# Optimization experiments

Hardware: AMD Instinct MI355X
Metric: run time of the kernel (lower is better)

The kernel has to match this reference:

```python
import jax, jax.numpy as jnp
import numpy as np
import math

D_MODEL = 1024
D_INNER = 2048
N_HEADS = 8
D_STATE = 64
D_CONV = 4
CHUNK = 64
HEAD_DIM = D_INNER // N_HEADS
EPS = 1.1920929e-07  # torch RMSNorm default eps = finfo(fp32).eps


def _rms(x, g):
    return x * jax.lax.rsqrt(jnp.mean(x * x, axis=-1, keepdims=True) + EPS) * g


def setup_inputs() -> dict:
    key = jax.random.key(0)
    ks = jax.random.split(key, 8)
    B, S = 32, 256
    proj_out = 2 * D_INNER + 2 * N_HEADS * D_STATE + N_HEADS  # 5128
    s = 0.02
    lambdas = [0.999, 0.995, 0.99, 0.98, 0.95, 0.9, 0.8, 0.7]
    A_log = jnp.log(jnp.asarray([-math.log(l) for l in lambdas], jnp.float32))
    return {
        "hidden": jax.random.normal(ks[0], (B, S, D_MODEL), jnp.float32),
        "W_in": jax.random.normal(ks[1], (proj_out, D_MODEL), jnp.float32) * s,
        "conv_w": jax.random.normal(ks[2], (D_INNER, 1, D_CONV), jnp.float32) * 0.2,
        "conv_b": jax.random.normal(ks[3], (D_INNER,), jnp.float32) * 0.02,
        "W_dt": jax.random.normal(ks[4], (D_INNER, N_HEADS), jnp.float32) * 0.1,
        "b_dt": jax.random.normal(ks[5], (D_INNER,), jnp.float32) * 0.1,
        "A_log": A_log,
        "D": jnp.ones((N_HEADS,), jnp.float32),
        "W_out": jax.random.normal(ks[6], (D_MODEL, D_INNER), jnp.float32) * s,
        "g_in": jnp.ones((D_MODEL,), jnp.float32),
        "g_out": jnp.ones((D_INNER,), jnp.float32),
    }


def reference(hidden, W_in, conv_w, conv_b, W_dt, b_dt, A_log, D, W_out, g_in, g_out):
    B, S, _ = hidden.shape
    residual = hidden
    h = _rms(hidden, g_in)
    proj = h @ W_in.T  # [B,S,5128]
    o1, o2 = D_INNER, 2 * D_INNER
    o3 = o2 + N_HEADS * D_STATE
    o4 = o3 + N_HEADS * D_STATE
    z = proj[..., :o1]
    x = proj[..., o1:o2]
    Bf = proj[..., o2:o3]
    Cf = proj[..., o3:o4]
    dt_raw = proj[..., o4:]
    # causal depthwise conv1d (pad left d_conv-1, trim to S)
    xt = jnp.transpose(x, (0, 2, 1))  # [B, d_inner, S]
    xc = jax.lax.conv_general_dilated(
        xt, conv_w, (1,), [(D_CONV - 1, 0)],
        feature_group_count=D_INNER, dimension_numbers=("NCH", "OIH", "NCH"))
    x = jax.nn.silu(jnp.transpose(xc + conv_b[None, :, None], (0, 2, 1)))
    # dt: project 8 -> d_inner then mean over head_dim -> per-head dt
    dt = dt_raw @ W_dt.T + b_dt  # [B,S,d_inner]
    dt_h = jax.nn.softplus(dt.reshape(B, S, N_HEADS, HEAD_DIM).mean(-1))  # non-TTT path (S<384)
    Bs = Bf.reshape(B, S, N_HEADS, D_STATE)
    Cs = Cf.reshape(B, S, N_HEADS, D_STATE)
    x_h = x.reshape(B, S, N_HEADS, HEAD_DIM)
    # chunked SSD scan
    A = -jnp.exp(A_log)  # [H]
    nC, L = S // CHUNK, CHUNK
    xck = x_h.reshape(B, nC, L, N_HEADS, HEAD_DIM)
    Bck = Bs.reshape(B, nC, L, N_HEADS, D_STATE)
    Cck = Cs.reshape(B, nC, L, N_HEADS, D_STATE)
    logA = dt_h.reshape(B, nC, L, N_HEADS) * A  # [B,c,L,H]
    lcs = jnp.cumsum(logA, axis=2)
    lcs_t = jnp.transpose(lcs, (0, 1, 3, 2))  # [B,c,H,L]
    tril = jnp.tril(jnp.ones((L, L), bool))
    M = jnp.where(tril, jnp.exp(lcs_t[..., :, None] - lcs_t[..., None, :]), 0.0)  # [B,c,H,L,L]
    # intra-chunk: sum_{s<=l,n} C[l,n] M[l,s] B[s,n] x[s,d]
    G = jnp.einsum("bclhn,bcshn->bchls", Cck, Bck)
    intra = jnp.einsum("bchls,bcshd->bclhd", G * M, xck)
    # per-chunk state contributions and decays
    Mlast = jnp.exp(lcs_t[..., -1:] - lcs_t)  # [B,c,H,L] decay from step s to chunk end
    states = jnp.einsum("bchs,bcshn,bcshd->bchdn", Mlast, Bck, xck)  # [B,c,H,hD,N]
    tdec = jnp.exp(lcs[:, :, -1, :])  # [B,c,H]
    def step(hst, inp):
        td, st = inp
        return td[..., None, None] * hst + st, hst
    init = jnp.zeros((B, N_HEADS, HEAD_DIM, D_STATE), x.dtype)
    _, h0 = jax.lax.scan(step, init, (jnp.moveaxis(tdec, 1, 0), jnp.moveaxis(states, 1, 0)))
    # inter-chunk: decay(l) * C[l] . h_start
    inter = jnp.exp(lcs)[..., None] * jnp.einsum("bclhn,cbhdn->bclhd", Cck, h0)
    y = (intra + inter).reshape(B, S, N_HEADS, HEAD_DIM) + x_h * D[None, None, :, None]
    y = y.reshape(B, S, D_INNER) * jax.nn.silu(z)
    y = _rms(y, g_out)
    return residual + y @ W_out.T
```

## Files before the change

kernel.cpp:

```cpp
#include <hip/hip_runtime.h>
#include <hip/hip_bf16.h>
#include <math.h>

typedef __hip_bfloat16 bf16;
typedef __attribute__((ext_vector_type(8))) short short8;
typedef __attribute__((ext_vector_type(4))) float f32x4;

#define AS1 __attribute__((address_space(1)))
#define AS3 __attribute__((address_space(3)))

#define D_MODEL 1024
#define D_INNER 2048
#define N_HEADS 8
#define D_STATE 64
#define CHUNK 64
#define HEAD_DIM 256
#define NCHUNK 4
#define BATCH 32
#define SEQ 256
#define ROWS (BATCH*SEQ)
#define PROJ_N 5128
#define PROJ_NPAD 5376
#define O1 D_INNER
#define O2 (2*D_INNER)
#define O3 (O2 + N_HEADS*D_STATE)
#define O4 (O3 + N_HEADS*D_STATE)
#define EPSF 1.1920929e-07f

__device__ __forceinline__ float silu_f(float x){ return x / (1.0f + expf(-x)); }
__device__ __forceinline__ float b2f(bf16 v){ return __bfloat162float(v); }
__device__ __forceinline__ bf16  f2b(float v){ return __float2bfloat16(v); }
__device__ __forceinline__ short f2s(float v){ bf16 b = __float2bfloat16(v); union{bf16 b; short s;} u; u.b=b; return u.s; }
__device__ __forceinline__ float s2f(short v){ union{short s; bf16 b;} u; u.s=v; return __bfloat162float(u.b); }

__device__ __forceinline__ void gl16(const void* g, void* l){
    __builtin_amdgcn_global_load_lds((const AS1 void*)g, (AS3 void*)l, 16, 0, 0);
}

__device__ __forceinline__ float block_sum_256(float v){
    __shared__ float sm[4];
    #pragma unroll
    for (int o = 32; o > 0; o >>= 1) v += __shfl_down(v, o, 64);
    int lane = threadIdx.x & 63, w = threadIdx.x >> 6;
    if (lane == 0) sm[w] = v;
    __syncthreads();
    return sm[0] + sm[1] + sm[2] + sm[3];
}

__global__ __launch_bounds__(256) void k_rms_in(const float* __restrict__ x,
                                                const float* __restrict__ g,
                                                bf16* __restrict__ out){
    int row = blockIdx.x, t = threadIdx.x;
    const float4* xr = (const float4*)(x + (size_t)row * D_MODEL);
    float4 v = xr[t];
    float ss = v.x*v.x + v.y*v.y + v.z*v.z + v.w*v.w;
    ss = block_sum_256(ss);
    float sc = rsqrtf(ss * (1.0f/(float)D_MODEL) + EPSF);
    float4 gv = ((const float4*)g)[t];
    union { ushort4 u; bf16 b[4]; } o;
    o.b[0] = f2b(v.x*sc*gv.x); o.b[1] = f2b(v.y*sc*gv.y);
    o.b[2] = f2b(v.z*sc*gv.z); o.b[3] = f2b(v.w*sc*gv.w);
    ((ushort4*)(out + (size_t)row * D_MODEL))[t] = o.u;
}

__global__ __launch_bounds__(256) void k_cvt_pad(const float* __restrict__ in,
                                                 bf16* __restrict__ out,
                                                 int n_in, int n_out){
    int i = (blockIdx.x * 256 + threadIdx.x) * 4;
    if (i >= n_out) return;
    union { ushort4 u; bf16 b[4]; } o;
    if (i + 3 < n_in){
        float4 v = *(const float4*)(in + i);
        o.b[0]=f2b(v.x); o.b[1]=f2b(v.y); o.b[2]=f2b(v.z); o.b[3]=f2b(v.w);
    } else {
        #pragma unroll
        for (int j = 0; j < 4; j++) o.b[j] = f2b((i+j < n_in) ? in[i+j] : 0.f);
    }
    *(ushort4*)(out + i) = o.u;
}


__device__ __forceinline__ short8 ld32(const short* base, int row, int g){
    int sr = row >> 1;
    int e8 = (((row & 1) << 2) | g) ^ (sr & 7);
    return *(const short8*)(base + sr*64 + e8*8);
}

__device__ __forceinline__ void stage_u(const bf16* __restrict__ Ag,
                                        const bf16* __restrict__ Bg,
                                        int K, size_t bm, size_t bn, int t,
                                        short* buf, int j){
    const int tid = threadIdx.x;
    const int wid = tid >> 6;
    int cidx = j*512 + tid;
    int srow = cidx >> 3, s8 = cidx & 7;
    int eff = s8 ^ (srow & 7);
    int grow = srow*2 + (eff >> 2);
    int gcol = t*32 + (eff & 3)*8;
    const bf16* src = (grow < 256)
        ? Ag + (bm + grow) * (size_t)K + gcol
        : Bg + (bn + grow - 256) * (size_t)K + gcol;
    gl16(src, buf + (size_t)(j*512 + wid*64)*8);
}

#define MFMA_BF16(A_,B_,C_) __builtin_amdgcn_mfma_f32_16x16x32_bf16(A_,B_,C_,0,0,0)

__device__ __forceinline__ void gemm_main(const bf16* __restrict__ Ag,
                                          const bf16* __restrict__ Bg,
                                          int K, size_t bm, size_t bn,
                                          short* lds, f32x4 (&acc)[4][4]){
    constexpr int TILE = 384*32;
    const int NT = K >> 5;
    const int lane = threadIdx.x & 63;
    const int wid = threadIdx.x >> 6;
    const int wm = wid >> 1, wn = wid & 1;
    const int fr = lane & 15, g = lane >> 4;

    #pragma unroll
    for (int j = 0; j < 3; j++) stage_u(Ag, Bg, K, bm, bn, 0, lds, j);
    #pragma unroll
    for (int j = 0; j < 3; j++) stage_u(Ag, Bg, K, bm, bn, 1, lds + TILE, j);
    asm volatile("s_waitcnt vmcnt(3)" ::: "memory");
    __builtin_amdgcn_sched_barrier(0);
    __builtin_amdgcn_s_barrier();
    __builtin_amdgcn_sched_barrier(0);

    int cur = 0;
    for (int t = 0; t < NT; t++){
        short* buf = lds + cur*TILE;
        int sg = cur + 2; if (sg >= 3) sg -= 3;
        short* stg = lds + sg*TILE;
        short8 a[4], b[4];
        #pragma unroll
        for (int m = 0; m < 4; m++) a[m] = ld32(buf, wm*64 + m*16 + fr, g);
        #pragma unroll
        for (int n = 0; n < 4; n++) b[n] = ld32(buf, 256 + wn*64 + n*16 + fr, g);
        if (t + 2 < NT){
            stage_u(Ag, Bg, K, bm, bn, t+2, stg, 0);
            stage_u(Ag, Bg, K, bm, bn, t+2, stg, 1);
            stage_u(Ag, Bg, K, bm, bn, t+2, stg, 2);
        }
        __builtin_amdgcn_s_setprio(1);
        #pragma unroll
        for (int m = 0; m < 4; m++)
            #pragma unroll
            for (int n = 0; n < 4; n++)
                acc[m][n] = MFMA_BF16(a[m], b[n], acc[m][n]);
        __builtin_amdgcn_s_setprio(0);
        __builtin_amdgcn_sched_barrier(0);
        if (t + 2 < NT)      asm volatile("s_waitcnt vmcnt(3)" ::: "memory");
        else if (t + 1 < NT) asm volatile("s_waitcnt vmcnt(0)" ::: "memory");
        __builtin_amdgcn_sched_barrier(0);
        __builtin_amdgcn_s_barrier();
        __builtin_amdgcn_sched_barrier(0);
        cur = cur + 1 == 3 ? 0 : cur + 1;
    }
}

__global__ __launch_bounds__(512, 4) void k_gemm1_g(const bf16* __restrict__ A,
                                                    const bf16* __restrict__ B,
                                                    bf16* __restrict__ z,
                                                    bf16* __restrict__ xp,
                                                    bf16* __restrict__ Bc,
                                                    bf16* __restrict__ Cc,
                                                    float* __restrict__ dtr){
    extern __shared__ short lds[];
    int wg = (blockIdx.x & 7)*168 + (blockIdx.x >> 3);
    int grp = wg / 192, rem = wg % 192;
    int nt_ = grp*6 + rem % 6;
    int mt_ = rem / 6;
    size_t bm = (size_t)mt_ * 256;
    size_t bn = (size_t)nt_ * 128;
    f32x4 acc[4][4] = {};
    gemm_main(A, B, D_MODEL, bm, bn, lds, acc);
    const int lane = threadIdx.x & 63;
    const int wid = threadIdx.x >> 6;
    const int wm = wid >> 1, wn = wid & 1;
    int cr = (lane >> 4)*4, cc = lane & 15;
    #pragma unroll
    for (int m = 0; m < 4; m++){
        size_t r0 = bm + wm*64 + m*16 + cr;
        #pragma unroll
        for (int n = 0; n < 4; n++){
            int c = (int)bn + wn*64 + n*16 + cc;
            #pragma unroll
            for (int j = 0; j < 4; j++){
                float v = acc[m][n][j];
                size_t r = r0 + j;
                if (c < O1)            z  [r * D_INNER + c]        = f2b(v);
                else if (c < O2)       xp [r * D_INNER + (c - O1)] = f2b(v);
                else if (c < O3)       Bc [r * 512 + (c - O2)]     = f2b(v);
                else if (c < O4)       Cc [r * 512 + (c - O3)]     = f2b(v);
                else if (c < PROJ_N)   dtr[r * 8 + (c - O4)]       = v;
            }
        }
    }
}

__global__ __launch_bounds__(512, 4) void k_gemm2_g(const bf16* __restrict__ A,
                                                    const bf16* __restrict__ B,
                                                    const float* __restrict__ res,
                                                    float* __restrict__ C){
    extern __shared__ short lds[];
    int wg = (blockIdx.x & 7)*32 + (blockIdx.x >> 3);
    size_t bm = (size_t)(wg >> 3) * 256;
    size_t bn = (size_t)(wg & 7) * 128;
    f32x4 acc[4][4] = {};
    gemm_main(A, B, D_INNER, bm, bn, lds, acc);
    const int lane = threadIdx.x & 63;
    const int wid = threadIdx.x >> 6;
    const int wm = wid >> 1, wn = wid & 1;
    int cr = (lane >> 4)*4, cc = lane & 15;
    #pragma unroll
    for (int m = 0; m < 4; m++){
        size_t r0 = bm + wm*64 + m*16 + cr;
        #pragma unroll
        for (int n = 0; n < 4; n++){
            size_t c = bn + wn*64 + n*16 + cc;
            #pragma unroll
            for (int j = 0; j < 4; j++){
                size_t r = r0 + j;
                C[r * D_MODEL + c] = acc[m][n][j] + res[r * D_MODEL + c];
            }
        }
    }
}

__global__ __launch_bounds__(256) void k_conv_silu(const bf16* __restrict__ xp,
                                                   const float* __restrict__ cw,
                                                   const float* __restrict__ cb,
                                                   bf16* __restrict__ xout){
    int b = blockIdx.x;
    int c = blockIdx.y * 256 + threadIdx.x;
    int s0 = blockIdx.z * 32;
    float w0 = cw[c*4+0], w1 = cw[c*4+1], w2 = cw[c*4+2], w3 = cw[c*4+3];
    float bias = cb[c];
    const bf16* ib = xp + (size_t)b * SEQ * D_INNER + c;
    bf16* ob = xout + (size_t)b * SEQ * D_INNER + c;
    float x0 = 0.f, x1 = 0.f, x2 = 0.f;
    if (s0 >= 3){
        x0 = b2f(ib[(size_t)(s0-3) * D_INNER]);
        x1 = b2f(ib[(size_t)(s0-2) * D_INNER]);
        x2 = b2f(ib[(size_t)(s0-1) * D_INNER]);
    }
    #pragma unroll 4
    for (int s = s0; s < s0 + 32; s++){
        float x3 = b2f(ib[(size_t)s * D_INNER]);
        float a = x0*w0 + x1*w1 + x2*w2 + x3*w3 + bias;
        ob[(size_t)s * D_INNER] = f2b(silu_f(a));
        x0 = x1; x1 = x2; x2 = x3;
    }
}

__global__ __launch_bounds__(64) void k_dt_lcs(const float* __restrict__ dtr,
                                               const float* __restrict__ W_dt,
                                               const float* __restrict__ b_dt,
                                               const float* __restrict__ A_log,
                                               float* __restrict__ lcs,
                                               float* __restrict__ tdec){
    __shared__ float sm[80];
    __shared__ float la[CHUNK][N_HEADS];
    int bc = blockIdx.x;
    int l = threadIdx.x;
    {
        int h = l >> 3, k = l & 7;
        float s = 0.f;
        for (int d = 0; d < HEAD_DIM; d++) s += W_dt[(size_t)(h*HEAD_DIM + d) * N_HEADS + k];
        sm[l] = s * (1.0f/(float)HEAD_DIM);
        if (l < 8){
            float sb = 0.f;
            for (int d = 0; d < HEAD_DIM; d++) sb += b_dt[l*HEAD_DIM + d];
            sm[64 + l] = sb * (1.0f/(float)HEAD_DIM);
            sm[72 + l] = -expf(A_log[l]);
        }
    }
    __syncthreads();
    const float* dr = dtr + (size_t)(bc*CHUNK + l) * 8;
    float d0 = dr[0], d1 = dr[1], d2 = dr[2], d3 = dr[3];
    float d4 = dr[4], d5 = dr[5], d6 = dr[6], d7 = dr[7];
    #pragma unroll
    for (int h = 0; h < 8; h++){
        float dt = sm[64+h]
                 + d0*sm[h*8+0] + d1*sm[h*8+1] + d2*sm[h*8+2] + d3*sm[h*8+3]
                 + d4*sm[h*8+4] + d5*sm[h*8+5] + d6*sm[h*8+6] + d7*sm[h*8+7];
        float sp = (dt > 20.f) ? dt : log1pf(expf(dt));
        la[l][h] = sp * sm[72+h];
    }
    __syncthreads();
    float out[8];
    #pragma unroll
    for (int h = 0; h < 8; h++) out[h] = 0.f;
    for (int l2 = 0; l2 <= l; l2++){
        #pragma unroll
        for (int h = 0; h < 8; h++) out[h] += la[l2][h];
    }
    float* lo = lcs + (size_t)(bc*CHUNK + l) * N_HEADS;
    #pragma unroll
    for (int h = 0; h < 8; h++) lo[h] = out[h];
    if (l == 63){
        #pragma unroll
        for (int h = 0; h < 8; h++) tdec[bc*N_HEADS + h] = expf(out[h]);
    }
}

#define LB   0
#define LC   4096
#define LGM  8192
#define LXT  12800
#define LSH  29184
#define LF   45568
#define LDS_BYTES 91904

__device__ __forceinline__ short8 frag_sw(const short* arr, int r, int k){
    return *(const short8*)(arr + r*64 + (k ^ ((r&7)<<3)));
}

__global__ __launch_bounds__(256, 1) void k_ssm(const bf16* __restrict__ Bc,
                                                const bf16* __restrict__ Cc,
                                                bf16* xg,
                                                const float* __restrict__ lcs,
                                                const float* __restrict__ tdec,
                                                const float* __restrict__ Dv){
    extern __shared__ short lds[];
    short* Blds  = lds + LB;
    short* Clds  = lds + LC;
    short* GMlds = lds + LGM;
    short* XTlds = lds + LXT;
    short* Shr   = lds + LSH;
    float* el = (float*)(lds + LF);
    float* ml = el + 64;
    float* ee = el + 128;

    const int tid = threadIdx.x;
    const int lane = tid & 63;
    const int wid = tid >> 6;
    const int fr = lane & 15;
    const int fk = (lane >> 4) * 8;
    const int r0 = (lane >> 4) * 4;
    const int b = blockIdx.x >> 3, h = blockIdx.x & 7;
    const float Dh = Dv[h];

    f32x4 carry[4][4] = {};

    for (int c = 0; c < NCHUNK; c++){
        const int bc = b*NCHUNK + c;
        __syncthreads();
        #pragma unroll
        for (int i = 0; i < 2; i++){
            int slot = i*256 + tid;
            int s = slot >> 3, u = slot & 7;
            size_t rb = (size_t)(bc*CHUNK + s) * 512 + h*64 + ((u ^ (s&7)) * 8);
            gl16(Bc + rb, Blds + slot*8);
            gl16(Cc + rb, Clds + slot*8);
        }
        #pragma unroll
        for (int i = 0; i < 8; i++){
            int slot = i*256 + tid;
            int s = slot >> 5, ck = slot & 31;
            gl16(xg + (size_t)(bc*CHUNK + s) * D_INNER + h*HEAD_DIM + ck*8, Shr + slot*8);
        }
        if (tid < 64) el[tid] = lcs[(size_t)(bc*CHUNK + tid) * N_HEADS + h];
        __syncthreads();
        if (tid < 64){
            float e63 = el[63];
            ml[tid] = expf(e63 - el[tid]);
            ee[tid] = expf(el[tid]);
        }
        #pragma unroll
        for (int i = 0; i < 8; i++){
            short8 t8;
            #pragma unroll
            for (int j = 0; j < 8; j++) t8[j] = Shr[(i*8 + j)*HEAD_DIM + tid];
            *(short8*)(XTlds + tid*64 + ((i*8) ^ ((tid&7)<<3))) = t8;
        }
        __syncthreads();
        {
            f32x4 accg[4] = {};
            #pragma unroll
            for (int kk = 0; kk < 2; kk++){
                short8 a = frag_sw(Clds, wid*16 + fr, kk*32 + fk);
                #pragma unroll
                for (int nt = 0; nt < 4; nt++){
                    short8 bb = frag_sw(Blds, nt*16 + fr, kk*32 + fk);
                    accg[nt] = __builtin_amdgcn_mfma_f32_16x16x32_bf16(a, bb, accg[nt], 0, 0, 0);
                }
            }
            #pragma unroll
            for (int nt = 0; nt < 4; nt++){
                int s = nt*16 + fr;
                float els = el[s];
                #pragma unroll
                for (int j = 0; j < 4; j++){
                    int l = wid*16 + r0 + j;
                    float f = (s <= l) ? expf(el[l] - els) : 0.f;
                    GMlds[l*72 + s] = f2s(accg[nt][j] * f);
                }
            }
            int crow = wid*16 + (lane >> 2), cq = lane & 3;
            float fe = ee[crow];
            #pragma unroll
            for (int half = 0; half < 2; half++){
                short8 v = *(short8*)(Clds + crow*64 + cq*16 + half*8);
                #pragma unroll
                for (int j = 0; j < 8; j++) v[j] = f2s(s2f(v[j]) * fe);
                *(short8*)(Clds + crow*64 + cq*16 + half*8) = v;
            }
        }
        #pragma unroll
        for (int mt = 0; mt < 4; mt++)
            #pragma unroll
            for (int nt = 0; nt < 4; nt++)
                #pragma unroll
                for (int j = 0; j < 4; j++){
                    int d = wid*64 + mt*16 + r0 + j;
                    int n = nt*16 + fr;
                    Shr[d*64 + (n ^ ((d&7)<<3))] = f2s(carry[mt][nt][j]);
                }
        float btv[16];
        {
            int bn_ = tid & 63, bq = tid >> 6;
            #pragma unroll
            for (int i = 0; i < 16; i++){
                int s = bq*16 + i;
                btv[i] = s2f(Blds[s*64 + (bn_ ^ ((s&7)<<3))]) * ml[s];
            }
        }
        __syncthreads();
        {
            int bn_ = tid & 63, bq = tid >> 6;
            #pragma unroll
            for (int i = 0; i < 16; i++){
                int s = bq*16 + i;
                Blds[bn_*64 + (s ^ ((bn_&7)<<3))] = f2s(btv[i]);
            }
        }
        {
            f32x4 accy[4][4] = {};
            #pragma unroll
            for (int kk = 0; kk < 2; kk++){
                short8 ag[4], ae[4], bx[4], bh[4];
                #pragma unroll
                for (int mt = 0; mt < 4; mt++){
                    ag[mt] = *(const short8*)(GMlds + (mt*16 + fr)*72 + kk*32 + fk);
                    ae[mt] = frag_sw(Clds, mt*16 + fr, kk*32 + fk);
                }
                #pragma unroll
                for (int nt = 0; nt < 4; nt++){
                    int d = wid*64 + nt*16 + fr;
                    bx[nt] = frag_sw(XTlds, d, kk*32 + fk);
                    bh[nt] = frag_sw(Shr,  d, kk*32 + fk);
                }
                #pragma unroll
                for (int mt = 0; mt < 4; mt++)
                    #pragma unroll
                    for (int nt = 0; nt < 4; nt++){
                        accy[mt][nt] = __builtin_amdgcn_mfma_f32_16x16x32_bf16(ag[mt], bx[nt], accy[mt][nt], 0, 0, 0);
                        accy[mt][nt] = __builtin_amdgcn_mfma_f32_16x16x32_bf16(ae[mt], bh[nt], accy[mt][nt], 0, 0, 0);
                    }
            }
            #pragma unroll
            for (int mt = 0; mt < 4; mt++)
                #pragma unroll
                for (int nt = 0; nt < 4; nt++){
                    int d = wid*64 + nt*16 + fr;
                    #pragma unroll
                    for (int j = 0; j < 4; j++){
                        int l = mt*16 + r0 + j;
                        float xv = s2f(XTlds[d*64 + (l ^ ((d&7)<<3))]);
                        xg[(size_t)(bc*CHUNK + l) * D_INNER + h*HEAD_DIM + d] = f2b(accy[mt][nt][j] + xv*Dh);
                    }
                }
        }
        __syncthreads();
        {
            f32x4 accs[4][4] = {};
            #pragma unroll
            for (int kk = 0; kk < 2; kk++){
                short8 ax[4], bt[4];
                #pragma unroll
                for (int mt = 0; mt < 4; mt++)
                    ax[mt] = frag_sw(XTlds, wid*64 + mt*16 + fr, kk*32 + fk);
                #pragma unroll
                for (int nt = 0; nt < 4; nt++)
                    bt[nt] = frag_sw(Blds, nt*16 + fr, kk*32 + fk);
                #pragma unroll
                for (int mt = 0; mt < 4; mt++)
                    #pragma unroll
                    for (int nt = 0; nt < 4; nt++)
                        accs[mt][nt] = __builtin_amdgcn_mfma_f32_16x16x32_bf16(ax[mt], bt[nt], accs[mt][nt], 0, 0, 0);
            }
            float td = tdec[bc*N_HEADS + h];
            #pragma unroll
            for (int mt = 0; mt < 4; mt++)
                #pragma unroll
                for (int nt = 0; nt < 4; nt++)
                    carry[mt][nt] = td * carry[mt][nt] + accs[mt][nt];
        }
    }
}

__global__ __launch_bounds__(256) void k_gate_rms(const bf16* __restrict__ y,
                                                  const bf16* __restrict__ z,
                                                  const float* __restrict__ g,
                                                  bf16* __restrict__ yn){
    int row = blockIdx.x, t = threadIdx.x;
    union { uint4 u; bf16 b[8]; } yv, zv, ov;
    yv.u = ((const uint4*)(y + (size_t)row * D_INNER))[t];
    zv.u = ((const uint4*)(z + (size_t)row * D_INNER))[t];
    float v[8];
    float ss = 0.f;
    #pragma unroll
    for (int i = 0; i < 8; i++){
        float a = b2f(yv.b[i]);
        float q = b2f(zv.b[i]);
        v[i] = a * silu_f(q);
        ss += v[i]*v[i];
    }
    ss = block_sum_256(ss);
    float sc = rsqrtf(ss * (1.0f/(float)D_INNER) + EPSF);
    const float4* g4 = (const float4*)g;
    float4 ga = g4[2*t], gb = g4[2*t+1];
    float gg[8] = {ga.x,ga.y,ga.z,ga.w,gb.x,gb.y,gb.z,gb.w};
    #pragma unroll
    for (int i = 0; i < 8; i++) ov.b[i] = f2b(v[i]*sc*gg[i]);
    ((uint4*)(yn + (size_t)row * D_INNER))[t] = ov.u;
}

extern "C" void kernel_launch(void* const* d_in, const int* in_sizes, int n_in,
                              void* d_out, int out_size, void* d_ws, size_t ws_size,
                              hipStream_t stream){
    const float* hidden = (const float*)d_in[0];
    const float* W_in   = (const float*)d_in[1];
    const float* conv_w = (const float*)d_in[2];
    const float* conv_b = (const float*)d_in[3];
    const float* W_dt   = (const float*)d_in[4];
    const float* b_dt   = (const float*)d_in[5];
    const float* A_log  = (const float*)d_in[6];
    const float* Dv     = (const float*)d_in[7];
    const float* W_out  = (const float*)d_in[8];
    const float* g_in   = (const float*)d_in[9];
    const float* g_out  = (const float*)d_in[10];

    char* ws = (char*)d_ws;
    bf16*  z    = (bf16*)(ws + 0);
    bf16*  xp   = (bf16*)(ws + 33554432);
    bf16*  x    = (bf16*)(ws + 67108864);
    bf16*  Bc   = (bf16*)(ws + 100663296);
    bf16*  Cc   = (bf16*)(ws + 109051904);
    float* dtr  = (float*)(ws + 117440512);
    float* lcs  = (float*)(ws + 117702656);
    float* tdec = (float*)(ws + 117964800);
    bf16*  Wb   = (bf16*)(ws + 117969408);
    bf16*  hnb  = (bf16*)(ws + 128979456);
    bf16*  yn   = xp;

    k_rms_in<<<ROWS, 256, 0, stream>>>(hidden, g_in, hnb);
    k_cvt_pad<<<(PROJ_NPAD*D_MODEL/4 + 255)/256, 256, 0, stream>>>(W_in, Wb, PROJ_N*D_MODEL, PROJ_NPAD*D_MODEL);
    hipFuncSetAttribute((const void*)k_gemm1_g, hipFuncAttributeMaxDynamicSharedMemorySize, 73728);
    k_gemm1_g<<<(ROWS/256)*(PROJ_NPAD/128), 512, 73728, stream>>>(hnb, Wb, z, xp, Bc, Cc, dtr);
    k_conv_silu<<<dim3(BATCH, D_INNER/256, SEQ/32), 256, 0, stream>>>(xp, conv_w, conv_b, x);
    k_dt_lcs<<<BATCH*NCHUNK, 64, 0, stream>>>(dtr, W_dt, b_dt, A_log, lcs, tdec);
    hipFuncSetAttribute((const void*)k_ssm, hipFuncAttributeMaxDynamicSharedMemorySize, LDS_BYTES);
    k_ssm<<<BATCH*N_HEADS, 256, LDS_BYTES, stream>>>(Bc, Cc, x, lcs, tdec, Dv);
    k_gate_rms<<<ROWS, 256, 0, stream>>>(x, z, g_out, yn);
    k_cvt_pad<<<(D_MODEL*D_INNER/4 + 255)/256, 256, 0, stream>>>(W_out, Wb, D_MODEL*D_INNER, D_MODEL*D_INNER);
    hipFuncSetAttribute((const void*)k_gemm2_g, hipFuncAttributeMaxDynamicSharedMemorySize, 73728);
    k_gemm2_g<<<(ROWS/256)*(D_MODEL/128), 512, 73728, stream>>>(yn, Wb, hidden, (float*)d_out);
}
```

Before: 266.8 us.

## Fuse gating into SSM, fold RMS scale into GEMM2, merge weight conversions

The silu(z) gate moves into the SSM epilogue. The output RMSNorm is split into two parts: a row-scale kernel that only computes rsqrt per row, and a g_out multiply folded into the bf16 W_out conversion, so the per-row scale is applied in the GEMM2 epilogue. This removes one full read-modify-write pass over the normalized activations. Both weight conversions are merged into one launch, and GEMM2 switches to a 4-stage LDS pipeline (prefetch depth 3) with more shared memory, which may lower occupancy. The sum of squares is now taken over bf16-rounded gated values, which slightly changes numerics.

```diff
diff --git a/kernel.cpp b/kernel.cpp
--- a/kernel.cpp
+++ b/kernel.cpp
@@ -63,20 +63,33 @@
     ((ushort4*)(out + (size_t)row * D_MODEL))[t] = o.u;
 }
 
-__global__ __launch_bounds__(256) void k_cvt_pad(const float* __restrict__ in,
-                                                 bf16* __restrict__ out,
-                                                 int n_in, int n_out){
+#define N1 (PROJ_NPAD*D_MODEL)
+__global__ __launch_bounds__(256) void k_cvt_both(const float* __restrict__ W_in,
+                                                  const float* __restrict__ W_out,
+                                                  const float* __restrict__ g_out,
+                                                  bf16* __restrict__ Wb1,
+                                                  bf16* __restrict__ Wb2){
     int i = (blockIdx.x * 256 + threadIdx.x) * 4;
-    if (i >= n_out) return;
     union { ushort4 u; bf16 b[4]; } o;
-    if (i + 3 < n_in){
-        float4 v = *(const float4*)(in + i);
-        o.b[0]=f2b(v.x); o.b[1]=f2b(v.y); o.b[2]=f2b(v.z); o.b[3]=f2b(v.w);
+    if (i < N1){
+        int n_in = PROJ_N*D_MODEL;
+        if (i + 3 < n_in){
+            float4 v = *(const float4*)(W_in + i);
+            o.b[0]=f2b(v.x); o.b[1]=f2b(v.y); o.b[2]=f2b(v.z); o.b[3]=f2b(v.w);
+        } else {
+            #pragma unroll
+            for (int j = 0; j < 4; j++) o.b[j] = f2b((i+j < n_in) ? W_in[i+j] : 0.f);
+        }
+        *(ushort4*)(Wb1 + i) = o.u;
     } else {
-        #pragma unroll
-        for (int j = 0; j < 4; j++) o.b[j] = f2b((i+j < n_in) ? in[i+j] : 0.f);
-    }
-    *(ushort4*)(out + i) = o.u;
+        int k2 = i - N1;
+        if (k2 < D_MODEL*D_INNER){
+            float4 v = *(const float4*)(W_out + k2);
+            float4 gv = *(const float4*)(g_out + (k2 & (D_INNER-1)));
+            o.b[0]=f2b(v.x*gv.x); o.b[1]=f2b(v.y*gv.y); o.b[2]=f2b(v.z*gv.z); o.b[3]=f2b(v.w*gv.w);
+            *(ushort4*)(Wb2 + k2) = o.u;
+        }
+    }
 }
 
 
@@ -154,6 +167,59 @@
         __builtin_amdgcn_s_barrier();
         __builtin_amdgcn_sched_barrier(0);
         cur = cur + 1 == 3 ? 0 : cur + 1;
+    }
+}
+
+__device__ __forceinline__ void gemm_main_r4(const bf16* __restrict__ Ag,
+                                             const bf16* __restrict__ Bg,
+                                             int K, size_t bm, size_t bn,
+                                             short* lds, f32x4 (&acc)[4][4]){
+    constexpr int TILE = 384*32;
+    const int NT = K >> 5;
+    const int lane = threadIdx.x & 63;
+    const int wid = threadIdx.x >> 6;
+    const int wm = wid >> 1, wn = wid & 1;
+    const int fr = lane & 15, g = lane >> 4;
+
+    #pragma unroll
+    for (int p = 0; p < 3; p++)
+        #pragma unroll
+        for (int j = 0; j < 3; j++) stage_u(Ag, Bg, K, bm, bn, p, lds + p*TILE, j);
+    asm volatile("s_waitcnt vmcnt(6)" ::: "memory");
+    __builtin_amdgcn_sched_barrier(0);
+    __builtin_amdgcn_s_barrier();
+    __builtin_amdgcn_sched_barrier(0);
+
+    int cur = 0;
+    for (int t = 0; t < NT; t++){
+        short* buf = lds + cur*TILE;
+        int sg = cur + 3; if (sg >= 4) sg -= 4;
+        short* stg = lds + sg*TILE;
+        short8 a[4], b[4];
+        #pragma unroll
+        for (int m = 0; m < 4; m++) a[m] = ld32(buf, wm*64 + m*16 + fr, g);
+        #pragma unroll
+        for (int n = 0; n < 4; n++) b[n] = ld32(buf, 256 + wn*64 + n*16 + fr, g);
+        if (t + 3 < NT){
+            stage_u(Ag, Bg, K, bm, bn, t+3, stg, 0);
+            stage_u(Ag, Bg, K, bm, bn, t+3, stg, 1);
+            stage_u(Ag, Bg, K, bm, bn, t+3, stg, 2);
+        }
+        __builtin_amdgcn_s_setprio(1);
+        #pragma unroll
+        for (int m = 0; m < 4; m++)
+            #pragma unroll
+            for (int n = 0; n < 4; n++)
+                acc[m][n] = MFMA_BF16(a[m], b[n], acc[m][n]);
+        __builtin_amdgcn_s_setprio(0);
+        __builtin_amdgcn_sched_barrier(0);
+        if (t + 3 < NT)      asm volatile("s_waitcnt vmcnt(6)" ::: "memory");
+        else if (t + 2 < NT) asm volatile("s_waitcnt vmcnt(3)" ::: "memory");
+        else if (t + 1 < NT) asm volatile("s_waitcnt vmcnt(0)" ::: "memory");
+        __builtin_amdgcn_sched_barrier(0);
+        __builtin_amdgcn_s_barrier();
+        __builtin_amdgcn_sched_barrier(0);
+        cur = cur + 1 == 4 ? 0 : cur + 1;
     }
 }
 
@@ -200,13 +266,14 @@
 __global__ __launch_bounds__(512, 4) void k_gemm2_g(const bf16* __restrict__ A,
                                                     const bf16* __restrict__ B,
                                                     const float* __restrict__ res,
+                                                    const float* __restrict__ sc,
                                                     float* __restrict__ C){
     extern __shared__ short lds[];
     int wg = (blockIdx.x & 7)*32 + (blockIdx.x >> 3);
     size_t bm = (size_t)(wg >> 3) * 256;
     size_t bn = (size_t)(wg & 7) * 128;
     f32x4 acc[4][4] = {};
-    gemm_main(A, B, D_INNER, bm, bn, lds, acc);
+    gemm_main_r4(A, B, D_INNER, bm, bn, lds, acc);
     const int lane = threadIdx.x & 63;
     const int wid = threadIdx.x >> 6;
     const int wm = wid >> 1, wn = wid & 1;
@@ -220,7 +287,7 @@
             #pragma unroll
             for (int j = 0; j < 4; j++){
                 size_t r = r0 + j;
-                C[r * D_MODEL + c] = acc[m][n][j] + res[r * D_MODEL + c];
+                C[r * D_MODEL + c] = acc[m][n][j]*sc[r] + res[r * D_MODEL + c];
             }
         }
     }
@@ -318,6 +385,7 @@
 __global__ __launch_bounds__(256, 1) void k_ssm(const bf16* __restrict__ Bc,
                                                 const bf16* __restrict__ Cc,
                                                 bf16* xg,
+                                                const bf16* __restrict__ zg,
                                                 const float* __restrict__ lcs,
                                                 const float* __restrict__ tdec,
                                                 const float* __restrict__ Dv){
@@ -467,7 +535,10 @@
                     for (int j = 0; j < 4; j++){
                         int l = mt*16 + r0 + j;
                         float xv = s2f(XTlds[d*64 + (l ^ ((d&7)<<3))]);
-                        xg[(size_t)(bc*CHUNK + l) * D_INNER + h*HEAD_DIM + d] = f2b(accy[mt][nt][j] + xv*Dh);
+                        size_t gi = (size_t)(bc*CHUNK + l) * D_INNER + h*HEAD_DIM + d;
+                        float yv = accy[mt][nt][j] + xv*Dh;
+                        float zv = b2f(zg[gi]);
+                        xg[gi] = f2b(yv * silu_f(zv));
                     }
                 }
         }
@@ -499,31 +570,19 @@
     }
 }
 
-__global__ __launch_bounds__(256) void k_gate_rms(const bf16* __restrict__ y,
-                                                  const bf16* __restrict__ z,
-                                                  const float* __restrict__ g,
-                                                  bf16* __restrict__ yn){
+__global__ __launch_bounds__(256) void k_rowsc(const bf16* __restrict__ yg,
+                                               float* __restrict__ sc){
     int row = blockIdx.x, t = threadIdx.x;
-    union { uint4 u; bf16 b[8]; } yv, zv, ov;
-    yv.u = ((const uint4*)(y + (size_t)row * D_INNER))[t];
-    zv.u = ((const uint4*)(z + (size_t)row * D_INNER))[t];
-    float v[8];
+    union { uint4 u; bf16 b[8]; } v;
+    v.u = ((const uint4*)(yg + (size_t)row * D_INNER))[t];
     float ss = 0.f;
     #pragma unroll
     for (int i = 0; i < 8; i++){
-        float a = b2f(yv.b[i]);
-        float q = b2f(zv.b[i]);
-        v[i] = a * silu_f(q);
-        ss += v[i]*v[i];
+        float a = b2f(v.b[i]);
+        ss += a*a;
     }
     ss = block_sum_256(ss);
-    float sc = rsqrtf(ss * (1.0f/(float)D_INNER) + EPSF);
-    const float4* g4 = (const float4*)g;
-    float4 ga = g4[2*t], gb = g4[2*t+1];
-    float gg[8] = {ga.x,ga.y,ga.z,ga.w,gb.x,gb.y,gb.z,gb.w};
-    #pragma unroll
-    for (int i = 0; i < 8; i++) ov.b[i] = f2b(v[i]*sc*gg[i]);
-    ((uint4*)(yn + (size_t)row * D_INNER))[t] = ov.u;
+    if (t == 0) sc[row] = rsqrtf(ss * (1.0f/(float)D_INNER) + EPSF);
 }
 
 extern "C" void kernel_launch(void* const* d_in, const int* in_sizes, int n_in,
@@ -550,20 +609,20 @@
     float* dtr  = (float*)(ws + 117440512);
     float* lcs  = (float*)(ws + 117702656);
     float* tdec = (float*)(ws + 117964800);
-    bf16*  Wb   = (bf16*)(ws + 117969408);
+    bf16*  Wb1  = (bf16*)(ws + 117969408);
     bf16*  hnb  = (bf16*)(ws + 128979456);
-    bf16*  yn   = xp;
+    bf16*  Wb2  = (bf16*)(ws + 145756672);
+    float* sc   = (float*)(ws + 149950976);
 
     k_rms_in<<<ROWS, 256, 0, stream>>>(hidden, g_in, hnb);
-    k_cvt_pad<<<(PROJ_NPAD*D_MODEL/4 + 255)/256, 256, 0, stream>>>(W_in, Wb, PROJ_N*D_MODEL, PROJ_NPAD*D_MODEL);
+    k_cvt_both<<<(N1 + D_MODEL*D_INNER)/1024, 256, 0, stream>>>(W_in, W_out, g_out, Wb1, Wb2);
     hipFuncSetAttribute((const void*)k_gemm1_g, hipFuncAttributeMaxDynamicSharedMemorySize, 73728);
-    k_gemm1_g<<<(ROWS/256)*(PROJ_NPAD/128), 512, 73728, stream>>>(hnb, Wb, z, xp, Bc, Cc, dtr);
+    k_gemm1_g<<<(ROWS/256)*(PROJ_NPAD/128), 512, 73728, stream>>>(hnb, Wb1, z, xp, Bc, Cc, dtr);
     k_conv_silu<<<dim3(BATCH, D_INNER/256, SEQ/32), 256, 0, stream>>>(xp, conv_w, conv_b, x);
     k_dt_lcs<<<BATCH*NCHUNK, 64, 0, stream>>>(dtr, W_dt, b_dt, A_log, lcs, tdec);
     hipFuncSetAttribute((const void*)k_ssm, hipFuncAttributeMaxDynamicSharedMemorySize, LDS_BYTES);
-    k_ssm<<<BATCH*N_HEADS, 256, LDS_BYTES, stream>>>(Bc, Cc, x, lcs, tdec, Dv);
-    k_gate_rms<<<ROWS, 256, 0, stream>>>(x, z, g_out, yn);
-    k_cvt_pad<<<(D_MODEL*D_INNER/4 + 255)/256, 256, 0, stream>>>(W_out, Wb, D_MODEL*D_INNER, D_MODEL*D_INNER);
-    hipFuncSetAttribute((const void*)k_gemm2_g, hipFuncAttributeMaxDynamicSharedMemorySize, 73728);
-    k_gemm2_g<<<(ROWS/256)*(D_MODEL/128), 512, 73728, stream>>>(yn, Wb, hidden, (float*)d_out);
-}
+    k_ssm<<<BATCH*N_HEADS, 256, LDS_BYTES, stream>>>(Bc, Cc, x, z, lcs, tdec, Dv);
+    k_rowsc<<<ROWS, 256, 0, stream>>>(x, sc);
+    hipFuncSetAttribute((const void*)k_gemm2_g, hipFuncAttributeMaxDynamicSharedMemorySize, 98304);
+    k_gemm2_g<<<(ROWS/256)*(D_MODEL/128), 512, 98304, stream>>>(x, Wb2, hidden, sc, (float*)d_out);
+}
```

Result: slower. 323.1 us (+21.1%).
